# Kernel tuning notes

Measured on AMD Instinct MI355X. Metric: run time of the kernel, lower is better.

## Reference

```python
import jax, jax.numpy as jnp
import numpy as np

N_ENTITY, N_REL, DIM, H = 500000, 32, 64, 2
N_ITEM, N_MEM, BATCH, HIST = 10000, 32, 4096, 50


def setup_inputs() -> dict:
    key = jax.random.key(0)
    ks = jax.random.split(key, 10)
    return {
        "entity_emb": jax.random.normal(ks[0], (N_ENTITY, DIM), jnp.float32) * 0.05,
        "relation_emb": jax.random.normal(ks[1], (N_REL, DIM), jnp.float32) * 0.05,
        "W_w": jax.random.normal(ks[2], (1, 3 * DIM), jnp.float32) * 0.05,
        "W_b": jnp.zeros((1,), jnp.float32),
        "item_ids": jax.random.randint(ks[3], (N_ITEM,), 0, N_ENTITY, jnp.int32),
        "heads": jax.random.randint(ks[4], (H, N_ITEM, N_MEM), 0, N_ENTITY, jnp.int32),
        "relations": jax.random.randint(ks[5], (H, N_ITEM, N_MEM), 0, N_REL, jnp.int32),
        "tails": jax.random.randint(ks[6], (H, N_ITEM, N_MEM), 0, N_ENTITY, jnp.int32),
        "records_idx": jax.random.randint(ks[7], (BATCH, HIST), 0, N_ITEM, jnp.int32),
        "items": jax.random.randint(ks[8], (BATCH,), 0, N_ENTITY, jnp.int32),
    }


def reference(entity_emb, relation_emb, W_w, W_b, item_ids, heads, relations, tails, records_idx, items):
    d = entity_emb.shape[1]
    # Split the Linear(3d->1) weight so we never materialize the [n_item,m,3d] concat.
    w_h, w_r, w_t = W_w[0, :d], W_w[0, d:2 * d], W_w[0, 2 * d:]
    # Hop-0 item embedding (base entity embedding of each candidate item).
    acc = entity_emb[item_ids]  # [n_item, d]
    for h in range(heads.shape[0]):
        te = entity_emb[tails[h]]  # [n_item, m, d]
        logits = (entity_emb[heads[h]] @ w_h
                  + relation_emb[relations[h]] @ w_r
                  + te @ w_t + W_b[0])  # [n_item, m]
        # Original: sigmoid then softmax over the memory axis.
        pi = jax.nn.softmax(jax.nn.sigmoid(logits), axis=1)[..., None]
        acc = acc + (pi * te).sum(axis=1)
    # User embedding = sum of (hop-enhanced) item embeddings over history records.
    user_emb = acc[records_idx].sum(axis=1)  # [B, d]
    pair_item = entity_emb[items]            # [B, d] (raw entity embedding)
    return jax.nn.sigmoid(jnp.sum(user_emb * pair_item, axis=-1))
```

## Files before the change

### kernel.cpp

```cpp
#include <hip/hip_runtime.h>
#include <math.h>

#define DIM    64
#define N_MEM  32
#define N_ITEM 10000
#define HOPS   2
#define BATCH  4096
#define HIST   50

__device__ __forceinline__ float wave_reduce_sum(float v) {
#pragma unroll
    for (int off = 32; off > 0; off >>= 1)
        v += __shfl_xor(v, off, 64);
    return v;
}

__global__ __launch_bounds__(256) void ripple_stage1(
    const float* __restrict__ entity_emb,
    const float* __restrict__ relation_emb,
    const float* __restrict__ W_w,
    const float* __restrict__ W_b,
    const int*   __restrict__ item_ids,
    const int*   __restrict__ heads,
    const int*   __restrict__ relations,
    const int*   __restrict__ tails,
    float*       __restrict__ acc_out)
{
    const int wave = (blockIdx.x * blockDim.x + threadIdx.x) >> 6;
    const int lane = threadIdx.x & 63;
    if (wave >= N_ITEM) return;
    const int i = __builtin_amdgcn_readfirstlane(wave);

    const float w_h  = W_w[lane];
    const float w_r  = W_w[DIM + lane];
    const float w_t  = W_w[2 * DIM + lane];
    const float bias = W_b[0];

    float acc = entity_emb[(size_t)item_ids[i] * DIM + lane];

#pragma unroll
    for (int h = 0; h < HOPS; ++h) {
        const int base = __builtin_amdgcn_readfirstlane((h * N_ITEM + i) * N_MEM);

        float part[N_MEM];
#pragma unroll
        for (int m = 0; m < N_MEM; ++m) {
            const float he = entity_emb[(size_t)heads[base + m] * DIM + lane];
            const float re = relation_emb[relations[base + m] * DIM + lane];
            const float te = entity_emb[(size_t)tails[base + m] * DIM + lane];
            part[m] = he * w_h + re * w_r + te * w_t;
        }

        float e[N_MEM];
        float sum_e = 0.f;
#pragma unroll
        for (int m = 0; m < N_MEM; ++m) {
            const float logit = wave_reduce_sum(part[m]) + bias;
            const float sig   = 1.f / (1.f + __expf(-logit));
            const float exm   = __expf(sig);
            e[m] = exm;
            sum_e += exm;
        }
        const float inv = 1.f / sum_e;

#pragma unroll
        for (int m = 0; m < N_MEM; ++m) {
            const float te = entity_emb[(size_t)tails[base + m] * DIM + lane];
            acc += (e[m] * inv) * te;
        }
    }
    acc_out[i * DIM + lane] = acc;
}

__global__ __launch_bounds__(256) void ripple_stage2(
    const float* __restrict__ entity_emb,
    const int*   __restrict__ records_idx,
    const int*   __restrict__ items,
    const float* __restrict__ acc_buf,
    float*       __restrict__ out)
{
    const int wave = (blockIdx.x * blockDim.x + threadIdx.x) >> 6;
    const int lane = threadIdx.x & 63;
    if (wave >= BATCH) return;
    const int b = __builtin_amdgcn_readfirstlane(wave);

    const int rbase = __builtin_amdgcn_readfirstlane(b * HIST);
    float user = 0.f;
#pragma unroll
    for (int j = 0; j < HIST; ++j)
        user += acc_buf[(size_t)records_idx[rbase + j] * DIM + lane];

    const float pair = entity_emb[(size_t)items[b] * DIM + lane];
    const float dot  = wave_reduce_sum(user * pair);
    if (lane == 0) out[b] = 1.f / (1.f + __expf(-dot));
}

extern "C" void kernel_launch(void* const* d_in, const int* in_sizes, int n_in,
                              void* d_out, int out_size, void* d_ws, size_t ws_size,
                              hipStream_t stream) {
    const float* entity_emb   = (const float*)d_in[0];
    const float* relation_emb = (const float*)d_in[1];
    const float* W_w          = (const float*)d_in[2];
    const float* W_b          = (const float*)d_in[3];
    const int*   item_ids     = (const int*)d_in[4];
    const int*   heads        = (const int*)d_in[5];
    const int*   relations    = (const int*)d_in[6];
    const int*   tails        = (const int*)d_in[7];
    const int*   records_idx  = (const int*)d_in[8];
    const int*   items        = (const int*)d_in[9];
    float* out = (float*)d_out;

    float* acc_buf = (float*)d_ws;

    const int blocks1 = (N_ITEM + 3) / 4;
    ripple_stage1<<<blocks1, 256, 0, stream>>>(entity_emb, relation_emb, W_w, W_b,
                                               item_ids, heads, relations, tails,
                                               acc_buf);

    const int blocks2 = (BATCH + 3) / 4;
    ripple_stage2<<<blocks2, 256, 0, stream>>>(entity_emb, records_idx, items,
                                               acc_buf, out);
}
```

Before: 253.5 us.

## Split each wave into four 16-lane groups using float4 row loads

Both kernels now treat a wave as four groups of 16 lanes. Each lane loads a float4 slice of an embedding row, so each group covers one row and the wave handles four memory slots or history records per step. This shortens the shuffle reductions from 6 steps to 4 for logits, adds cross-group reductions at the end, and caches tail embeddings in registers instead of re-gathering them. In exchange, the index loads are no longer wave-uniform, the register footprint grows, and the 50-record loop is padded to 52 with masked dummy loads.

```diff
diff --git a/kernel.cpp b/kernel.cpp
--- a/kernel.cpp
+++ b/kernel.cpp
@@ -8,12 +8,8 @@
 #define BATCH  4096
 #define HIST   50
 
-__device__ __forceinline__ float wave_reduce_sum(float v) {
-#pragma unroll
-    for (int off = 32; off > 0; off >>= 1)
-        v += __shfl_xor(v, off, 64);
-    return v;
-}
+typedef float4 f4;
+
 
 __global__ __launch_bounds__(256) void ripple_stage1(
     const float* __restrict__ entity_emb,
@@ -29,47 +25,82 @@
     const int wave = (blockIdx.x * blockDim.x + threadIdx.x) >> 6;
     const int lane = threadIdx.x & 63;
     if (wave >= N_ITEM) return;
-    const int i = __builtin_amdgcn_readfirstlane(wave);
+    const int g = lane >> 4;
+    const int p = lane & 15;
 
-    const float w_h  = W_w[lane];
-    const float w_r  = W_w[DIM + lane];
-    const float w_t  = W_w[2 * DIM + lane];
+    const f4* __restrict__ E4 = (const f4*)entity_emb;
+    const f4* __restrict__ R4 = (const f4*)relation_emb;
+    const f4* __restrict__ W4 = (const f4*)W_w;
+
+    const f4 wh = W4[p];
+    const f4 wr = W4[16 + p];
+    const f4 wt = W4[32 + p];
     const float bias = W_b[0];
 
-    float acc = entity_emb[(size_t)item_ids[i] * DIM + lane];
+    f4 acc = {0.f, 0.f, 0.f, 0.f};
+    {
+        const f4 it = E4[(size_t)item_ids[wave] * 16 + p];
+        if (g == 0) acc = it;
+    }
 
 #pragma unroll
     for (int h = 0; h < HOPS; ++h) {
-        const int base = __builtin_amdgcn_readfirstlane((h * N_ITEM + i) * N_MEM);
+        const int base = (h * N_ITEM + wave) * N_MEM + g;
 
-        float part[N_MEM];
+        f4    te[8];
+        float part[8];
 #pragma unroll
-        for (int m = 0; m < N_MEM; ++m) {
-            const float he = entity_emb[(size_t)heads[base + m] * DIM + lane];
-            const float re = relation_emb[relations[base + m] * DIM + lane];
-            const float te = entity_emb[(size_t)tails[base + m] * DIM + lane];
-            part[m] = he * w_h + re * w_r + te * w_t;
+        for (int k = 0; k < 8; ++k) {
+            const int hi = heads[base + 4 * k];
+            const int ri = relations[base + 4 * k];
+            const int ti = tails[base + 4 * k];
+            const f4 he = E4[(size_t)hi * 16 + p];
+            const f4 re = R4[(size_t)ri * 16 + p];
+            const f4 t  = E4[(size_t)ti * 16 + p];
+            te[k] = t;
+            part[k] = he.x * wh.x + he.y * wh.y + he.z * wh.z + he.w * wh.w
+                    + re.x * wr.x + re.y * wr.y + re.z * wr.z + re.w * wr.w
+                    + t.x  * wt.x + t.y  * wt.y + t.z  * wt.z + t.w  * wt.w;
         }
 
-        float e[N_MEM];
-        float sum_e = 0.f;
+        float e[8];
+        float se = 0.f;
 #pragma unroll
-        for (int m = 0; m < N_MEM; ++m) {
-            const float logit = wave_reduce_sum(part[m]) + bias;
+        for (int k = 0; k < 8; ++k) {
+            float v = part[k];
+            v += __shfl_xor(v, 1, 64);
+            v += __shfl_xor(v, 2, 64);
+            v += __shfl_xor(v, 4, 64);
+            v += __shfl_xor(v, 8, 64);
+            const float logit = v + bias;
             const float sig   = 1.f / (1.f + __expf(-logit));
-            const float exm   = __expf(sig);
-            e[m] = exm;
-            sum_e += exm;
+            const float ex    = __expf(sig);
+            e[k] = ex;
+            se += ex;
         }
-        const float inv = 1.f / sum_e;
+        se += __shfl_xor(se, 16, 64);
+        se += __shfl_xor(se, 32, 64);
+        const float inv = 1.f / se;
 
 #pragma unroll
-        for (int m = 0; m < N_MEM; ++m) {
-            const float te = entity_emb[(size_t)tails[base + m] * DIM + lane];
-            acc += (e[m] * inv) * te;
+        for (int k = 0; k < 8; ++k) {
+            const float w = e[k] * inv;
+            acc.x += w * te[k].x;
+            acc.y += w * te[k].y;
+            acc.z += w * te[k].z;
+            acc.w += w * te[k].w;
         }
     }
-    acc_out[i * DIM + lane] = acc;
+
+    acc.x += __shfl_xor(acc.x, 16, 64);
+    acc.x += __shfl_xor(acc.x, 32, 64);
+    acc.y += __shfl_xor(acc.y, 16, 64);
+    acc.y += __shfl_xor(acc.y, 32, 64);
+    acc.z += __shfl_xor(acc.z, 16, 64);
+    acc.z += __shfl_xor(acc.z, 32, 64);
+    acc.w += __shfl_xor(acc.w, 16, 64);
+    acc.w += __shfl_xor(acc.w, 32, 64);
+    if (g == 0) ((f4*)acc_out)[(size_t)wave * 16 + p] = acc;
 }
 
 __global__ __launch_bounds__(256) void ripple_stage2(
@@ -82,16 +113,42 @@
     const int wave = (blockIdx.x * blockDim.x + threadIdx.x) >> 6;
     const int lane = threadIdx.x & 63;
     if (wave >= BATCH) return;
-    const int b = __builtin_amdgcn_readfirstlane(wave);
+    const int b = wave;
+    const int g = lane >> 4;
+    const int p = lane & 15;
 
-    const int rbase = __builtin_amdgcn_readfirstlane(b * HIST);
-    float user = 0.f;
+    const f4* __restrict__ A4 = (const f4*)acc_buf;
+    const f4* __restrict__ E4 = (const f4*)entity_emb;
+
+    f4 user = {0.f, 0.f, 0.f, 0.f};
+    const int rb = b * HIST;
 #pragma unroll
-    for (int j = 0; j < HIST; ++j)
-        user += acc_buf[(size_t)records_idx[rbase + j] * DIM + lane];
+    for (int k = 0; k < 13; ++k) {
+        const int j  = 4 * k + g;
+        const int jc = j < HIST ? j : (HIST - 1);
+        const float w = j < HIST ? 1.f : 0.f;
+        const int idx = records_idx[rb + jc];
+        const f4 r = A4[(size_t)idx * 16 + p];
+        user.x += w * r.x;
+        user.y += w * r.y;
+        user.z += w * r.z;
+        user.w += w * r.w;
+    }
+    user.x += __shfl_xor(user.x, 16, 64);
+    user.x += __shfl_xor(user.x, 32, 64);
+    user.y += __shfl_xor(user.y, 16, 64);
+    user.y += __shfl_xor(user.y, 32, 64);
+    user.z += __shfl_xor(user.z, 16, 64);
+    user.z += __shfl_xor(user.z, 32, 64);
+    user.w += __shfl_xor(user.w, 16, 64);
+    user.w += __shfl_xor(user.w, 32, 64);
 
-    const float pair = entity_emb[(size_t)items[b] * DIM + lane];
-    const float dot  = wave_reduce_sum(user * pair);
+    const f4 pair = E4[(size_t)items[b] * 16 + p];
+    float dot = user.x * pair.x + user.y * pair.y + user.z * pair.z + user.w * pair.w;
+    dot += __shfl_xor(dot, 1, 64);
+    dot += __shfl_xor(dot, 2, 64);
+    dot += __shfl_xor(dot, 4, 64);
+    dot += __shfl_xor(dot, 8, 64);
     if (lane == 0) out[b] = 1.f / (1.f + __expf(-dot));
 }
 
```

Result: faster. 229.5 us (-9.5%).
